# Kernel optimization log

Measured on AMD Instinct MI355X. Metric: run time of the kernel, lower is better.

The kernel has to match this reference:

```python
import jax, jax.numpy as jnp
import numpy as np

D_MODEL = 1024
NUM_HEADS = 16
DEPTH = D_MODEL // NUM_HEADS  # 64
BATCH, SEQ = 4, 2048


def setup_inputs() -> dict:
    key = jax.random.key(0)
    ks = jax.random.split(key, 9)
    s = 1.0 / np.sqrt(D_MODEL)
    x = jax.random.normal(ks[0], (BATCH, SEQ, D_MODEL), dtype=jnp.float32)
    # Per-head Dense weights stacked on a leading head axis [H, d_model, depth]
    Wq = jax.random.normal(ks[1], (NUM_HEADS, D_MODEL, DEPTH), dtype=jnp.float32) * s
    Wk = jax.random.normal(ks[2], (NUM_HEADS, D_MODEL, DEPTH), dtype=jnp.float32) * s
    Wv = jax.random.normal(ks[3], (NUM_HEADS, D_MODEL, DEPTH), dtype=jnp.float32) * s
    bq = jnp.zeros((NUM_HEADS, DEPTH), dtype=jnp.float32)
    bk = jnp.zeros((NUM_HEADS, DEPTH), dtype=jnp.float32)
    bv = jnp.zeros((NUM_HEADS, DEPTH), dtype=jnp.float32)
    Wo = jax.random.normal(ks[4], (D_MODEL, D_MODEL), dtype=jnp.float32) * s
    bo = jnp.zeros((D_MODEL,), dtype=jnp.float32)
    return {"x": x, "Wq": Wq, "bq": bq, "Wk": Wk, "bk": bk,
            "Wv": Wv, "bv": bv, "Wo": Wo, "bo": bo}


def reference(x, Wq, bq, Wk, bk, Wv, bv, Wo, bo):
    # Batched equivalent of the per-head loop: project, attend, concat heads.
    q = jnp.einsum('bsd,hde->bhse', x, Wq) + bq[:, None, :]  # [B,H,S,depth]
    k = jnp.einsum('bsd,hde->bhse', x, Wk) + bk[:, None, :]
    v = jnp.einsum('bsd,hde->bhse', x, Wv) + bv[:, None, :]
    scale = 1.0 / jnp.sqrt(jnp.asarray(DEPTH, dtype=x.dtype))
    scores = jnp.einsum('bhse,bhte->bhst', q, k) * scale      # [B,H,S,S]
    weights = jax.nn.softmax(scores, axis=-1)
    heads = jnp.einsum('bhst,bhte->bhse', weights, v)         # [B,H,S,depth]
    # concat head outputs along last axis in head order (tf.concat axis=-1)
    multi = jnp.transpose(heads, (0, 2, 1, 3)).reshape(x.shape[0], x.shape[1], D_MODEL)
    return multi @ Wo + bo
```

## Files before the change

kernel.cpp:

```cpp
#include <hip/hip_runtime.h>
#include <hip/hip_bf16.h>

#define BATCH 4
#define SEQ   2048
#define DM    1024
#define NH    16
#define DEPTH 64
#define ROWS  (BATCH*SEQ)
#define NQKV  (3*DM)
#define BH    (BATCH*NH)

typedef __attribute__((ext_vector_type(8))) short bf16x8;
typedef __attribute__((ext_vector_type(4))) float f32x4;
typedef __attribute__((ext_vector_type(16))) float f32x16;
typedef unsigned short u16;
typedef unsigned int   u32;

__device__ __forceinline__ u16 f2bf(float f) {
    union { float f; unsigned u; } v; v.f = f;
    unsigned r = v.u + 0x7fff + ((v.u >> 16) & 1);
    return (u16)(r >> 16);
}

__device__ __forceinline__ u32 pk2bf(float a, float b) {
#if __has_builtin(__builtin_amdgcn_cvt_pk_bf16_f32)
    typedef __attribute__((ext_vector_type(2))) __bf16 v2bf;
    union { v2bf v; u32 u; } u_;
    u_.v = __builtin_amdgcn_cvt_pk_bf16_f32(a, b);
    return u_.u;
#else
    return (u32)f2bf(a) | ((u32)f2bf(b) << 16);
#endif
}

__device__ __forceinline__ void plswap(u32 a, u32 b, u32& x, u32& y) {
#if __has_builtin(__builtin_amdgcn_permlane32_swap)
    typedef __attribute__((ext_vector_type(2))) int i32x2;
    i32x2 r = __builtin_amdgcn_permlane32_swap((int)a, (int)b, false, false);
    x = (u32)r.x; y = (u32)r.y;
#else
    u32 as = (u32)__shfl_xor((int)a, 32);
    u32 bs = (u32)__shfl_xor((int)b, 32);
    int h = (threadIdx.x >> 5) & 1;
    x = h ? bs : a;
    y = h ? b : as;
#endif
}

__device__ __forceinline__ void g2l16(void* lds, const void* g) {
    __builtin_amdgcn_global_load_lds((const __attribute__((address_space(1))) void*)g,
                                     (__attribute__((address_space(3))) void*)lds, 16, 0, 0);
}

__device__ __forceinline__ bf16x8 frag8(const u16* tile, int row, int gl) {
    return *(const bf16x8*)(tile + row * 64 + ((gl ^ (row & 7)) * 8));
}

__device__ __forceinline__ f32x16 mfma32(bf16x8 a, bf16x8 b, f32x16 c) {
    return __builtin_amdgcn_mfma_f32_32x32x16_bf16(a, b, c, 0, 0, 0);
}

__global__ __launch_bounds__(256) void k_prep(const float* __restrict__ x,
                                              const float* __restrict__ Wq, const float* __restrict__ Wk,
                                              const float* __restrict__ Wv, const float* __restrict__ Wo,
                                              u16* __restrict__ xb, u16* __restrict__ BT, u16* __restrict__ WoT) {
    __shared__ u16 T[64][65];
    int tid = threadIdx.x;
    int bx = blockIdx.x;
    if (bx < 2048) {
        int i = bx * 4096 + tid * 4;
        for (int l = 0; l < 4; ++l) {
            float4 v = *(const float4*)(x + i + l * 1024);
            ushort4 o; o.x = f2bf(v.x); o.y = f2bf(v.y); o.z = f2bf(v.z); o.w = f2bf(v.w);
            *(ushort4*)(xb + i + l * 1024) = o;
        }
        return;
    }
    if (bx < 2816) {
        int q = bx - 2048;
        int kt = q & 15, mh = q >> 4, m = mh >> 4, h = mh & 15;
        const float* W = (m == 0) ? Wq : (m == 1) ? Wk : Wv;
        const float* src = W + ((size_t)h * 1024 + kt * 64) * 64;
        int e = tid & 63, r0 = tid >> 6;
        for (int i = 0; i < 16; ++i) { int r = i * 4 + r0; T[r][e] = f2bf(src[r * 64 + e]); }
        __syncthreads();
        int kk = tid & 63, e0 = tid >> 6;
        u16* dst = BT + ((size_t)m * 1024 + h * 64) * 1024 + kt * 64;
        for (int i = 0; i < 16; ++i) { int ee = i * 4 + e0; dst[ee * 1024 + kk] = T[kk][ee]; }
        return;
    }
    {
        int q = bx - 2816;
        int kt = q & 15, nt = q >> 4;
        const float* src = Wo + (size_t)kt * 64 * 1024 + nt * 64;
        int c = tid & 63, r0 = tid >> 6;
        for (int i = 0; i < 16; ++i) { int r = i * 4 + r0; T[r][c] = f2bf(src[r * 1024 + c]); }
        __syncthreads();
        int kk = tid & 63, e0 = tid >> 6;
        u16* dst = WoT + (size_t)nt * 64 * 1024 + kt * 64;
        for (int i = 0; i < 16; ++i) { int ee = i * 4 + e0; dst[ee * 1024 + kk] = T[kk][ee]; }
    }
}

__global__ __launch_bounds__(256, 2) void k_gemm_qkv(const u16* __restrict__ xb, const u16* __restrict__ Wt,
                                                     const float* __restrict__ bq, const float* __restrict__ bk,
                                                     const float* __restrict__ bv,
                                                     u16* __restrict__ Q, u16* __restrict__ K, u16* __restrict__ VT) {
    __shared__ u16 Al[2][128 * 64];
    __shared__ u16 Bl[2][128 * 64];
    int tid = threadIdx.x;
    int wave = tid >> 6, lane = tid & 63, l31 = lane & 31, h2 = lane >> 5;
    int wr = wave >> 1, wc = wave & 1;

    int b = blockIdx.x;
    int wg = (b & 7) * 192 + (b >> 3);

    bool isvt = (wg >= 1024);
    int row0, col0;
    const u16 *Am, *Bm;
    if (!isvt) {
        row0 = (wg >> 4) * 128; col0 = (wg & 15) * 128;
        Am = xb + (size_t)row0 * 1024;
        Bm = Wt + (size_t)col0 * 1024;
    } else {
        int b2 = wg - 1024;
        row0 = (b2 >> 6) * 128; col0 = (b2 & 63) * 128;
        Am = Wt + (size_t)(2048 + row0) * 1024;
        Bm = xb + (size_t)col0 * 1024;
    }

    f32x16 acc[2][2] = {};

    int sr[4], sgs[4], sdst[4];
#pragma unroll
    for (int l = 0; l < 4; ++l) {
        int idx = tid + l * 256;
        sr[l] = idx >> 3; sgs[l] = ((idx & 7) ^ (sr[l] & 7)) * 8; sdst[l] = idx * 8;
    }

#define QKV_STAGE(bufi, k0) \
    { _Pragma("unroll") for (int l = 0; l < 4; ++l) { \
        g2l16(&Al[bufi][sdst[l]], Am + sr[l] * 1024 + (k0) + sgs[l]); \
        g2l16(&Bl[bufi][sdst[l]], Bm + sr[l] * 1024 + (k0) + sgs[l]); } }

#define QKV_COMPUTE(bufi) \
    { _Pragma("unroll") for (int kk = 0; kk < 4; ++kk) { \
        bf16x8 a_[2], bb_[2]; \
        _Pragma("unroll") for (int mi = 0; mi < 2; ++mi) a_[mi] = frag8(Al[bufi], wr * 64 + mi * 32 + l31, 2 * kk + h2); \
        _Pragma("unroll") for (int ni = 0; ni < 2; ++ni) bb_[ni] = frag8(Bl[bufi], wc * 64 + ni * 32 + l31, 2 * kk + h2); \
        _Pragma("unroll") for (int mi = 0; mi < 2; ++mi) \
        _Pragma("unroll") for (int ni = 0; ni < 2; ++ni) \
            acc[mi][ni] = mfma32(a_[mi], bb_[ni], acc[mi][ni]); } }

    QKV_STAGE(0, 0)
    QKV_STAGE(1, 64)

    for (int t = 0; t < 15; ++t) {
        int cur = t & 1;
        asm volatile("s_waitcnt vmcnt(8)" ::: "memory");
        __builtin_amdgcn_s_barrier();
        asm volatile("" ::: "memory");
        __builtin_amdgcn_s_setprio(1);
        QKV_COMPUTE(cur)
        __builtin_amdgcn_s_setprio(0);
        asm volatile("" ::: "memory");
        __builtin_amdgcn_s_barrier();
        if (t < 14) QKV_STAGE(cur, (t + 2) * 64)
    }
    asm volatile("s_waitcnt vmcnt(0)" ::: "memory");
    __builtin_amdgcn_s_barrier();
    asm volatile("" ::: "memory");
    QKV_COMPUTE(1)
#undef QKV_STAGE
#undef QKV_COMPUTE

    if (!isvt) {
        const float QSCALE = 0.125f * 1.4426950408889634f;
        int m = (col0 >= 1024);
        const float* bias = m ? bk : bq;
        u16* dst0 = m ? K : Q;
#pragma unroll
        for (int ni = 0; ni < 2; ++ni) {
            int c = col0 + wc * 64 + ni * 32 + l31;
            int h = (c >> 6) & 15, e = c & 63;
            float bval = bias[h * 64 + e];
#pragma unroll
            for (int mi = 0; mi < 2; ++mi)
#pragma unroll
                for (int reg = 0; reg < 16; ++reg) {
                    int rowg = row0 + wr * 64 + mi * 32 + (reg & 3) + 8 * (reg >> 2) + 4 * h2;
                    int b_ = rowg >> 11, s = rowg & 2047;
                    int bh = b_ * 16 + h;
                    float v = acc[mi][ni][reg] + bval;
                    if (!m) v *= QSCALE;
                    dst0[((size_t)bh * 2048 + s) * 64 + e] = f2bf(v);
                }
        }
    } else {
#pragma unroll
        for (int ni = 0; ni < 2; ++ni) {
            int c = col0 + wc * 64 + ni * 32 + l31;
            int b_ = c >> 11, s = c & 2047;
#pragma unroll
            for (int mi = 0; mi < 2; ++mi)
#pragma unroll
                for (int reg = 0; reg < 16; ++reg) {
                    int ii = row0 + wr * 64 + mi * 32 + (reg & 3) + 8 * (reg >> 2) + 4 * h2;
                    float v = acc[mi][ni][reg] + bv[ii];
                    VT[((size_t)b_ * 1024 + ii) * 2048 + s] = f2bf(v);
                }
        }
    }
}

__global__ __launch_bounds__(256, 4) void k_attn(const u16* __restrict__ Q, const u16* __restrict__ K,
                                                 const u16* __restrict__ VT, u16* __restrict__ A2) {
    __shared__ u16 Kl[2][64 * 64];
    __shared__ u16 Vl[2][64 * 64];
    __shared__ float linv[128];
    int tid = threadIdx.x;
    int wave = tid >> 6, lane = tid & 63, l31 = lane & 31, h = lane >> 5;
    int bh = blockIdx.y;
    int m0 = blockIdx.x * 128;
    const u16* Qb = Q + (size_t)bh * 2048 * 64;
    const u16* Kb = K + (size_t)bh * 2048 * 64;
    const u16* Vb = VT + (size_t)bh * 64 * 2048;

    const u16* kp[2]; const u16* vp[2]; int dsti[2];
    for (int l = 0; l < 2; ++l) {
        int idx = tid + l * 256, r = idx >> 3, gs = ((idx & 7) ^ (r & 7)) * 8;
        dsti[l] = idx * 8;
        kp[l] = Kb + r * 64 + gs;
        vp[l] = Vb + r * 2048 + gs;
    }

    bf16x8 qb[4];
    {
        const u16* q0 = Qb + (size_t)(m0 + wave * 32 + l31) * 64 + h * 8;
#pragma unroll
        for (int s = 0; s < 4; ++s) qb[s] = *(const bf16x8*)(q0 + s * 16);
    }

    for (int l = 0; l < 2; ++l) { g2l16(&Kl[0][dsti[l]], kp[l]); g2l16(&Vl[0][dsti[l]], vp[l]); }
    __syncthreads();

    f32x16 oacc[2] = {};
    float lsum = 0.f;

    for (int t = 0; t < 32; ++t) {
        int cur = t & 1;
        if (t < 31) {
            for (int l = 0; l < 2; ++l) {
                g2l16(&Kl[cur ^ 1][dsti[l]], kp[l] + (t + 1) * 4096);
                g2l16(&Vl[cur ^ 1][dsti[l]], vp[l] + (t + 1) * 64);
            }
        }

        f32x16 sc[2] = {};
        __builtin_amdgcn_s_setprio(1);
#pragma unroll
        for (int s = 0; s < 4; ++s) {
            bf16x8 kf0 = frag8(Kl[cur], l31,      2 * s + h);
            bf16x8 kf1 = frag8(Kl[cur], 32 + l31, 2 * s + h);
            sc[0] = mfma32(kf0, qb[s], sc[0]);
            sc[1] = mfma32(kf1, qb[s], sc[1]);
        }
        __builtin_amdgcn_s_setprio(0);

        bf16x8 pa[4];
        float sq = 0.f;
#pragma unroll
        for (int kt = 0; kt < 2; ++kt)
#pragma unroll
            for (int gp = 0; gp < 2; ++gp) {
                float e00 = __builtin_amdgcn_exp2f(sc[kt][(2 * gp) * 4 + 0]);
                float e01 = __builtin_amdgcn_exp2f(sc[kt][(2 * gp) * 4 + 1]);
                float e02 = __builtin_amdgcn_exp2f(sc[kt][(2 * gp) * 4 + 2]);
                float e03 = __builtin_amdgcn_exp2f(sc[kt][(2 * gp) * 4 + 3]);
                float e10 = __builtin_amdgcn_exp2f(sc[kt][(2 * gp + 1) * 4 + 0]);
                float e11 = __builtin_amdgcn_exp2f(sc[kt][(2 * gp + 1) * 4 + 1]);
                float e12 = __builtin_amdgcn_exp2f(sc[kt][(2 * gp + 1) * 4 + 2]);
                float e13 = __builtin_amdgcn_exp2f(sc[kt][(2 * gp + 1) * 4 + 3]);
                sq += ((e00 + e01) + (e02 + e03)) + ((e10 + e11) + (e12 + e13));
                u32 ue = pk2bf(e00, e01), ve = pk2bf(e02, e03);
                u32 uo = pk2bf(e10, e11), vo = pk2bf(e12, e13);
                u32 w0, w1, w2, w3;
                plswap(ue, uo, w0, w2);
                plswap(ve, vo, w1, w3);
                union { bf16x8 v; u32 w[4]; } pu;
                pu.w[0] = w0; pu.w[1] = w1; pu.w[2] = w2; pu.w[3] = w3;
                pa[2 * kt + gp] = pu.v;
            }
        lsum += sq;

        __builtin_amdgcn_s_setprio(1);
#pragma unroll
        for (int s = 0; s < 4; ++s) {
            bf16x8 bv0 = frag8(Vl[cur], l31,      2 * s + h);
            bf16x8 bv1 = frag8(Vl[cur], 32 + l31, 2 * s + h);
            oacc[0] = mfma32(pa[s], bv0, oacc[0]);
            oacc[1] = mfma32(pa[s], bv1, oacc[1]);
        }
        __builtin_amdgcn_s_setprio(0);

        __syncthreads();
    }

    {
        float l2 = lsum + __shfl_xor(lsum, 32);
        linv[wave * 32 + l31] = 1.0f / l2;
    }
    int b_ = bh >> 4, hh = bh & 15;
    for (int g = 0; g < 4; ++g) {
        f32x4 iv = *(f32x4*)&linv[wave * 32 + 8 * g + 4 * h];
        for (int dt = 0; dt < 2; ++dt)
            for (int r = 0; r < 4; ++r) {
                int row = b_ * 2048 + m0 + wave * 32 + 8 * g + 4 * h + r;
                A2[row * 1024 + hh * 64 + dt * 32 + l31] = f2bf(oacc[dt][g * 4 + r] * iv[r]);
            }
    }
}

__global__ __launch_bounds__(256, 2) void k_gemm_out(const u16* __restrict__ A, const u16* __restrict__ BT,
                                                     const float* __restrict__ bo, float* __restrict__ out) {
    __shared__ u16 Al[2][128 * 64];
    __shared__ u16 Bl[2][128 * 64];
    int tid = threadIdx.x;
    int wave = tid >> 6, lane = tid & 63, l31 = lane & 31, h2 = lane >> 5;
    int wr = wave >> 1, wc = wave & 1;

    int b = blockIdx.x;
    int wg = (b & 7) * 64 + (b >> 3);
    int row0 = (wg >> 3) * 128, col0 = (wg & 7) * 128;

    const u16* Am = A  + (size_t)row0 * 1024;
    const u16* Bm = BT + (size_t)col0 * 1024;

    f32x16 acc[2][2] = {};

    int sr[4], sgs[4], sdst[4];
#pragma unroll
    for (int l = 0; l < 4; ++l) {
        int idx = tid + l * 256;
        sr[l] = idx >> 3; sgs[l] = ((idx & 7) ^ (sr[l] & 7)) * 8; sdst[l] = idx * 8;
    }

#define OUT_STAGE(bufi, k0) \
    { _Pragma("unroll") for (int l = 0; l < 4; ++l) { \
        g2l16(&Al[bufi][sdst[l]], Am + sr[l] * 1024 + (k0) + sgs[l]); \
        g2l16(&Bl[bufi][sdst[l]], Bm + sr[l] * 1024 + (k0) + sgs[l]); } }

#define OUT_COMPUTE(bufi) \
    { _Pragma("unroll") for (int kk = 0; kk < 4; ++kk) { \
        bf16x8 a_[2], bb_[2]; \
        _Pragma("unroll") for (int mi = 0; mi < 2; ++mi) a_[mi] = frag8(Al[bufi], wr * 64 + mi * 32 + l31, 2 * kk + h2); \
        _Pragma("unroll") for (int ni = 0; ni < 2; ++ni) bb_[ni] = frag8(Bl[bufi], wc * 64 + ni * 32 + l31, 2 * kk + h2); \
        _Pragma("unroll") for (int mi = 0; mi < 2; ++mi) \
        _Pragma("unroll") for (int ni = 0; ni < 2; ++ni) \
            acc[mi][ni] = mfma32(a_[mi], bb_[ni], acc[mi][ni]); } }

    OUT_STAGE(0, 0)
    OUT_STAGE(1, 64)

    for (int t = 0; t < 15; ++t) {
        int cur = t & 1;
        asm volatile("s_waitcnt vmcnt(8)" ::: "memory");
        __builtin_amdgcn_s_barrier();
        asm volatile("" ::: "memory");
        __builtin_amdgcn_s_setprio(1);
        OUT_COMPUTE(cur)
        __builtin_amdgcn_s_setprio(0);
        asm volatile("" ::: "memory");
        __builtin_amdgcn_s_barrier();
        if (t < 14) OUT_STAGE(cur, (t + 2) * 64)
    }
    asm volatile("s_waitcnt vmcnt(0)" ::: "memory");
    __builtin_amdgcn_s_barrier();
    asm volatile("" ::: "memory");
    OUT_COMPUTE(1)
#undef OUT_STAGE
#undef OUT_COMPUTE

#pragma unroll
    for (int ni = 0; ni < 2; ++ni) {
        int c = col0 + wc * 64 + ni * 32 + l31;
        float bias = bo[c];
#pragma unroll
        for (int mi = 0; mi < 2; ++mi)
#pragma unroll
            for (int reg = 0; reg < 16; ++reg) {
                int rowg = row0 + wr * 64 + mi * 32 + (reg & 3) + 8 * (reg >> 2) + 4 * h2;
                out[(size_t)rowg * 1024 + c] = acc[mi][ni][reg] + bias;
            }
    }
}

extern "C" void kernel_launch(void* const* d_in, const int* in_sizes, int n_in,
                              void* d_out, int out_size, void* d_ws, size_t ws_size,
                              hipStream_t stream) {
    const float* x  = (const float*)d_in[0];
    const float* Wq = (const float*)d_in[1];
    const float* bq = (const float*)d_in[2];
    const float* Wk = (const float*)d_in[3];
    const float* bk = (const float*)d_in[4];
    const float* Wv = (const float*)d_in[5];
    const float* bv = (const float*)d_in[6];
    const float* Wo = (const float*)d_in[7];
    const float* bo = (const float*)d_in[8];
    float* out = (float*)d_out;

    char* ws = (char*)d_ws;
    u16* xb    = (u16*)ws; ws += (size_t)ROWS * DM * 2;
    u16* WqkvT = (u16*)ws; ws += (size_t)NQKV * DM * 2;
    u16* WoT   = (u16*)ws; ws += (size_t)DM * DM * 2;
    u16* Qb    = (u16*)ws; ws += (size_t)BH * SEQ * DEPTH * 2;
    u16* Kb    = (u16*)ws; ws += (size_t)BH * SEQ * DEPTH * 2;
    u16* VTb   = (u16*)ws; ws += (size_t)BH * SEQ * DEPTH * 2;
    u16* A2    = xb;
    (void)ws_size;

    k_prep     <<<dim3(3072),   dim3(256), 0, stream>>>(x, Wq, Wk, Wv, Wo, xb, WqkvT, WoT);
    k_gemm_qkv <<<dim3(1536),   dim3(256), 0, stream>>>(xb, WqkvT, bq, bk, bv, Qb, Kb, VTb);
    k_attn     <<<dim3(16, 64), dim3(256), 0, stream>>>(Qb, Kb, VTb, A2);
    k_gemm_out <<<dim3(512),    dim3(256), 0, stream>>>(A2, WoT, bo, out);
}
```

Measured before the change: 301.0 us.

## Software-pipeline PV matmul one tile behind QK in attention loop

Restructures the attention inner loop so that the P·V MFMAs for the previous KV tile run right after the current tile's QK^T MFMAs, with the softmax exponentials following. The V prefetch is split out and issued after a mid-iteration barrier, and __syncthreads is replaced with explicit vmcnt waits and s_barrier. The goal is to overlap the exp/pack work with matrix-core work and to keep V buffer reuse safe. It adds a drain step after the loop, plus more live registers and a more delicate synchronization scheme.

```diff
diff --git a/kernel.cpp b/kernel.cpp
--- a/kernel.cpp
+++ b/kernel.cpp
@@ -242,18 +242,19 @@
     }
 
     for (int l = 0; l < 2; ++l) { g2l16(&Kl[0][dsti[l]], kp[l]); g2l16(&Vl[0][dsti[l]], vp[l]); }
-    __syncthreads();
+    asm volatile("s_waitcnt vmcnt(0)" ::: "memory");
+    __builtin_amdgcn_s_barrier();
+    asm volatile("" ::: "memory");
 
     f32x16 oacc[2] = {};
     float lsum = 0.f;
+    bf16x8 pa[4] = {};
 
     for (int t = 0; t < 32; ++t) {
-        int cur = t & 1;
+        int cur = t & 1, nxt = cur ^ 1;
+
         if (t < 31) {
-            for (int l = 0; l < 2; ++l) {
-                g2l16(&Kl[cur ^ 1][dsti[l]], kp[l] + (t + 1) * 4096);
-                g2l16(&Vl[cur ^ 1][dsti[l]], vp[l] + (t + 1) * 64);
-            }
+            for (int l = 0; l < 2; ++l) g2l16(&Kl[nxt][dsti[l]], kp[l] + (t + 1) * 4096);
         }
 
         f32x16 sc[2] = {};
@@ -265,9 +266,25 @@
             sc[0] = mfma32(kf0, qb[s], sc[0]);
             sc[1] = mfma32(kf1, qb[s], sc[1]);
         }
+        if (t > 0) {
+#pragma unroll
+            for (int s = 0; s < 4; ++s) {
+                bf16x8 bv0 = frag8(Vl[nxt], l31,      2 * s + h);
+                bf16x8 bv1 = frag8(Vl[nxt], 32 + l31, 2 * s + h);
+                oacc[0] = mfma32(pa[s], bv0, oacc[0]);
+                oacc[1] = mfma32(pa[s], bv1, oacc[1]);
+            }
+        }
         __builtin_amdgcn_s_setprio(0);
 
-        bf16x8 pa[4];
+        asm volatile("" ::: "memory");
+        __builtin_amdgcn_s_barrier();
+        asm volatile("" ::: "memory");
+
+        if (t < 31) {
+            for (int l = 0; l < 2; ++l) g2l16(&Vl[nxt][dsti[l]], vp[l] + (t + 1) * 64);
+        }
+
         float sq = 0.f;
 #pragma unroll
         for (int kt = 0; kt < 2; ++kt)
@@ -293,17 +310,19 @@
             }
         lsum += sq;
 
-        __builtin_amdgcn_s_setprio(1);
-#pragma unroll
-        for (int s = 0; s < 4; ++s) {
-            bf16x8 bv0 = frag8(Vl[cur], l31,      2 * s + h);
-            bf16x8 bv1 = frag8(Vl[cur], 32 + l31, 2 * s + h);
-            oacc[0] = mfma32(pa[s], bv0, oacc[0]);
-            oacc[1] = mfma32(pa[s], bv1, oacc[1]);
-        }
-        __builtin_amdgcn_s_setprio(0);
-
-        __syncthreads();
+        if (t < 31) {
+            asm volatile("s_waitcnt vmcnt(0)" ::: "memory");
+            __builtin_amdgcn_s_barrier();
+            asm volatile("" ::: "memory");
+        }
+    }
+
+#pragma unroll
+    for (int s = 0; s < 4; ++s) {
+        bf16x8 bv0 = frag8(Vl[1], l31,      2 * s + h);
+        bf16x8 bv1 = frag8(Vl[1], 32 + l31, 2 * s + h);
+        oacc[0] = mfma32(pa[s], bv0, oacc[0]);
+        oacc[1] = mfma32(pa[s], bv1, oacc[1]);
     }
 
     {
```

Measured after the change: 289.8 us. 3.7% less time.
